# Performance work log

Hardware: AMD Instinct MI355X
Metric: run time of the kernel (lower is better)

Reference implementation:

```python
import jax, jax.numpy as jnp
import numpy as np

N = 16384      # nodes
E = 524288     # edges (avg degree 32)
F_IN = 128     # input features
H1 = 256       # first_gcn_dimensions
H2 = 256       # second_gcn_dimensions
D1 = 64        # first_dense_neurons
D2 = 2         # second_dense_neurons (fixed by EYE=ones(2))


def setup_inputs() -> dict:
    key = jax.random.key(0)
    ks = jax.random.split(key, 8)
    w = lambda k, shp: (jax.random.normal(k, shp, jnp.float32) * 0.05)
    return dict(
        features=jax.random.normal(ks[0], (N, F_IN), jnp.float32),
        edges=jax.random.randint(ks[1], (2, E), 0, N),
        W1=w(ks[2], (F_IN, H1)), b1=jnp.zeros((H1,), jnp.float32),
        W2=w(ks[3], (H1, H2)), b2=jnp.zeros((H2,), jnp.float32),
        fc1_w=w(ks[4], (D1, H2)), fc1_b=jnp.zeros((D1,), jnp.float32),
        fc2_w=w(ks[5], (D2, D1)), fc2_b=jnp.zeros((D2,), jnp.float32),
    )


def gcn_conv(x, W, b, src, dst, n):
    """PyG GCNConv: xW, add self-loops, symmetric D^-1/2 (A+I) D^-1/2 aggregation."""
    x = x @ W
    loops = jnp.arange(n)
    s = jnp.concatenate([src, loops])
    d = jnp.concatenate([dst, loops])
    deg = jax.ops.segment_sum(jnp.ones(s.shape, x.dtype), d, num_segments=n)
    dinv = jnp.where(deg > 0, jax.lax.rsqrt(deg), 0.0)
    msg = x[s] * (dinv[s] * dinv[d])[:, None]          # gather + scale
    return jax.ops.segment_sum(msg, d, num_segments=n) + b  # scatter-add


def reference(features, edges, W1, b1, W2, b2, fc1_w, fc1_b, fc2_w, fc2_b):
    n = features.shape[0]
    src, dst = edges[0], edges[1]
    h1 = jax.nn.relu(gcn_conv(features, W1, b1, src, dst, n))
    h2 = gcn_conv(h1, W2, b2, src, dst, n)                 # [N, H2]
    a1 = jnp.tanh(h2 @ fc1_w.T + fc1_b)                    # [N, D1]
    assignment = jax.nn.softmax(a1 @ fc2_w.T + fc2_b, axis=1)  # [N, 2]
    group_features = assignment.T @ h2                     # [2, H2]
    # to_dense_adj: dense NxN adjacency, duplicate edges accumulate
    adj = jnp.zeros((n, n), h2.dtype).at[src, dst].add(1.0)
    new_adj = assignment.T @ (adj @ assignment)            # [2, 2]
    positive = jnp.clip(group_features[0][None, :], -100.0, 100.0)
    negative = jnp.clip(group_features[1][None, :], -100.0, 100.0)
    # F.normalize(p=1, dim=1) with eps=1e-12
    denom = jnp.maximum(jnp.sum(jnp.abs(new_adj), axis=1, keepdims=True), 1e-12)
    norm_diag = jnp.diag(new_adj / denom)
    pos_penalty = jnp.mean((norm_diag - 1.0) ** 2)         # MSE vs ones(2)
    graph_embedding = jnp.mean(group_features, axis=0, keepdims=True)  # [1, H2]
    return (graph_embedding, positive, negative, pos_penalty)
```

## Files before the change

kernel.cpp:

```cpp
#include <hip/hip_runtime.h>
#include <hip/hip_bf16.h>
#include <math.h>

#define N_NODES 16384
#define N_EDGES 524288
#define F_IN 128
#define H1 256
#define H2 256
#define D1 64
#define NA_GRID 512
#define DEG_CAP 96

typedef __attribute__((ext_vector_type(8))) short short8;
typedef __attribute__((ext_vector_type(4))) float floatx4;
typedef unsigned short ushort_t;
typedef unsigned int uint_t;

__device__ inline float bf2f(ushort_t u) {
    union { uint_t i; float f; } v;
    v.i = ((uint_t)u) << 16;
    return v.f;
}
__device__ inline ushort_t f2bs(float x) {
    __hip_bfloat16 h = __float2bfloat16(x);
    return *reinterpret_cast<ushort_t*>(&h);
}

__global__ __launch_bounds__(256) void hist_kernel(
    const int* __restrict__ dst, int* __restrict__ cnt) {
    int e = blockIdx.x * 256 + threadIdx.x;
    atomicAdd(&cnt[dst[e]], 1);
}

__global__ __launch_bounds__(256) void prep_fill(
    const int* __restrict__ src, const int* __restrict__ dst,
    const float* __restrict__ features, const float* __restrict__ W1,
    const float* __restrict__ W2, const float* __restrict__ fc1_w,
    const int* __restrict__ cnt, int* __restrict__ cur,
    int* __restrict__ col, ushort_t* __restrict__ z,
    ushort_t* __restrict__ W1t, ushort_t* __restrict__ W2t,
    ushort_t* __restrict__ fc1bf, float* __restrict__ dinv) {
    int b = blockIdx.x, t = threadIdx.x;
    if (b < 2048) {
        int e = b * 256 + t;
        int d = dst[e];
        int pos = atomicAdd(&cur[d], 1);
        if (pos < DEG_CAP) col[d * DEG_CAP + pos] = src[e];
    } else if (b < 4096) {
        int idx = ((b - 2048) * 256 + t) * 4;
        float di = rsqrtf((float)(cnt[idx >> 7] + 1));
        float4 v = *(const float4*)&features[idx];
        uint_t lo = (uint_t)f2bs(v.x * di) | ((uint_t)f2bs(v.y * di) << 16);
        uint_t hi = (uint_t)f2bs(v.z * di) | ((uint_t)f2bs(v.w * di) << 16);
        uint2 p; p.x = lo; p.y = hi;
        *(uint2*)&z[idx] = p;
    } else if (b < 4224) {
        int idx = (b - 4096) * 256 + t;
        int n = idx >> 7, k = idx & 127;
        W1t[idx] = f2bs(W1[k * 256 + n]);
    } else if (b < 4480) {
        int idx = (b - 4224) * 256 + t;
        int n = idx >> 8, k = idx & 255;
        W2t[idx] = f2bs(W2[k * 256 + n]);
    } else if (b < 4544) {
        int idx = (b - 4480) * 256 + t;
        fc1bf[idx] = f2bs(fc1_w[idx]);
    } else {
        int n = (b - 4544) * 256 + t;
        dinv[n] = rsqrtf((float)(cnt[n] + 1));
    }
}

__global__ __launch_bounds__(256) void fused_layer1(
    const ushort_t* __restrict__ zfeat, const int* __restrict__ cnt,
    const int* __restrict__ col, const float* __restrict__ dinv,
    const float* __restrict__ b1, const ushort_t* __restrict__ W1t,
    const ushort_t* __restrict__ W2t, ushort_t* __restrict__ bufY) {
    __shared__ __align__(16) ushort_t Az[16 * 136];
    __shared__ __align__(16) ushort_t Ah[16 * 264];
    const int tid = threadIdx.x;
    const int lane = tid & 63;
    const int wave = tid >> 6;
    const int m = lane & 15;
    const int quad = lane >> 4;
    const int row0 = blockIdx.x * 16;

    for (int ii = 0; ii < 4; ++ii) {
        const int nl = wave * 4 + ii;
        const int node = __builtin_amdgcn_readfirstlane(row0 + nl);
        const int foff = lane * 2;
        uint_t self = *(const uint_t*)&zfeat[(size_t)node * 128 + foff];
        float a0 = bf2f((ushort_t)(self & 0xffff));
        float a1 = bf2f((ushort_t)(self >> 16));
        const int s0 = node * DEG_CAP;
        const int s1 = s0 + min(cnt[node], DEG_CAP);
        int base = s0;
        for (; base + 8 <= s1; base += 8) {
            uint_t uu[8];
            #pragma unroll
            for (int q = 0; q < 8; ++q) {
                int j = col[base + q];
                uu[q] = *(const uint_t*)&zfeat[(size_t)j * 128 + foff];
            }
            #pragma unroll
            for (int q = 0; q < 8; ++q) {
                a0 += bf2f((ushort_t)(uu[q] & 0xffff));
                a1 += bf2f((ushort_t)(uu[q] >> 16));
            }
        }
        for (; base < s1; ++base) {
            int j = col[base];
            uint_t u = *(const uint_t*)&zfeat[(size_t)j * 128 + foff];
            a0 += bf2f((ushort_t)(u & 0xffff));
            a1 += bf2f((ushort_t)(u >> 16));
        }
        float di = dinv[node];
        *(uint_t*)&Az[nl * 136 + foff] =
            (uint_t)f2bs(a0 * di) | ((uint_t)f2bs(a1 * di) << 16);
    }
    __syncthreads();

    const int wcol0 = wave * 64;
    floatx4 acc[4];
    const floatx4 zero4 = {0.f, 0.f, 0.f, 0.f};
    #pragma unroll
    for (int j = 0; j < 4; ++j) acc[j] = zero4;
    #pragma unroll
    for (int k0 = 0; k0 < 128; k0 += 32) {
        short8 a = *(const short8*)&Az[m * 136 + k0 + quad * 8];
        #pragma unroll
        for (int j = 0; j < 4; ++j) {
            short8 bb = *(const short8*)
                &W1t[(size_t)(wcol0 + j * 16 + m) * 128 + k0 + quad * 8];
            acc[j] = __builtin_amdgcn_mfma_f32_16x16x32_bf16(a, bb, acc[j], 0, 0, 0);
        }
    }
    #pragma unroll
    for (int j = 0; j < 4; ++j) {
        int cg = wcol0 + j * 16 + m;
        float bv = b1[cg];
        #pragma unroll
        for (int r = 0; r < 4; ++r) {
            float v = fmaxf(acc[j][r] + bv, 0.0f);
            Ah[(quad * 4 + r) * 264 + cg] = f2bs(v);
        }
    }
    __syncthreads();

    #pragma unroll
    for (int j = 0; j < 4; ++j) acc[j] = zero4;
    #pragma unroll
    for (int k0 = 0; k0 < 256; k0 += 32) {
        short8 a = *(const short8*)&Ah[m * 264 + k0 + quad * 8];
        #pragma unroll
        for (int j = 0; j < 4; ++j) {
            short8 bb = *(const short8*)
                &W2t[(size_t)(wcol0 + j * 16 + m) * 256 + k0 + quad * 8];
            acc[j] = __builtin_amdgcn_mfma_f32_16x16x32_bf16(a, bb, acc[j], 0, 0, 0);
        }
    }
    float rs4[4];
    #pragma unroll
    for (int r = 0; r < 4; ++r) rs4[r] = dinv[row0 + quad * 4 + r];
    #pragma unroll
    for (int j = 0; j < 4; ++j) {
        int cg = wcol0 + j * 16 + m;
        #pragma unroll
        for (int r = 0; r < 4; ++r)
            bufY[(size_t)(row0 + quad * 4 + r) * 256 + cg] = f2bs(acc[j][r] * rs4[r]);
    }
}

__global__ __launch_bounds__(256) void fused_assign(
    const ushort_t* __restrict__ bufY, const int* __restrict__ cnt,
    const int* __restrict__ col, const float* __restrict__ dinv,
    const float* __restrict__ b2, const ushort_t* __restrict__ fc1bf,
    const float* __restrict__ fc1_b, const float* __restrict__ fc2_w,
    const float* __restrict__ fc2_b, float* __restrict__ assign,
    float* __restrict__ gfr) {
    __shared__ __align__(16) ushort_t Ah[16 * 264];
    __shared__ float sha[16][65];
    __shared__ float sas0[16], sas1[16];
    const int tid = threadIdx.x;
    const int lane = tid & 63;
    const int wave = tid >> 6;
    const int m = lane & 15;
    const int quad = lane >> 4;
    const int row0 = blockIdx.x * 16;

    for (int ii = 0; ii < 4; ++ii) {
        const int nl = wave * 4 + ii;
        const int node = __builtin_amdgcn_readfirstlane(row0 + nl);
        const int foff = lane * 4;
        float a0, a1, a2, a3;
        {
            uint2 u = *(const uint2*)&bufY[(size_t)node * 256 + foff];
            a0 = bf2f((ushort_t)(u.x & 0xffff));
            a1 = bf2f((ushort_t)(u.x >> 16));
            a2 = bf2f((ushort_t)(u.y & 0xffff));
            a3 = bf2f((ushort_t)(u.y >> 16));
        }
        const int s0 = node * DEG_CAP;
        const int s1 = s0 + min(cnt[node], DEG_CAP);
        int base = s0;
        for (; base + 8 <= s1; base += 8) {
            uint2 uu[8];
            #pragma unroll
            for (int q = 0; q < 8; ++q) {
                int j = col[base + q];
                uu[q] = *(const uint2*)&bufY[(size_t)j * 256 + foff];
            }
            #pragma unroll
            for (int q = 0; q < 8; ++q) {
                a0 += bf2f((ushort_t)(uu[q].x & 0xffff));
                a1 += bf2f((ushort_t)(uu[q].x >> 16));
                a2 += bf2f((ushort_t)(uu[q].y & 0xffff));
                a3 += bf2f((ushort_t)(uu[q].y >> 16));
            }
        }
        for (; base < s1; ++base) {
            int j = col[base];
            uint2 u = *(const uint2*)&bufY[(size_t)j * 256 + foff];
            a0 += bf2f((ushort_t)(u.x & 0xffff));
            a1 += bf2f((ushort_t)(u.x >> 16));
            a2 += bf2f((ushort_t)(u.y & 0xffff));
            a3 += bf2f((ushort_t)(u.y >> 16));
        }
        float di = dinv[node];
        uint2 pk;
        pk.x = (uint_t)f2bs(a0 * di + b2[foff + 0]) |
               ((uint_t)f2bs(a1 * di + b2[foff + 1]) << 16);
        pk.y = (uint_t)f2bs(a2 * di + b2[foff + 2]) |
               ((uint_t)f2bs(a3 * di + b2[foff + 3]) << 16);
        *(uint2*)&Ah[nl * 264 + foff] = pk;
    }
    __syncthreads();

    floatx4 acc = {0.f, 0.f, 0.f, 0.f};
    #pragma unroll
    for (int k0 = 0; k0 < 256; k0 += 32) {
        short8 a = *(const short8*)&Ah[m * 264 + k0 + quad * 8];
        short8 bb = *(const short8*)
            &fc1bf[(size_t)(wave * 16 + m) * 256 + k0 + quad * 8];
        acc = __builtin_amdgcn_mfma_f32_16x16x32_bf16(a, bb, acc, 0, 0, 0);
    }
    {
        int cg = wave * 16 + m;
        float bv = fc1_b[cg];
        #pragma unroll
        for (int r = 0; r < 4; ++r)
            sha[quad * 4 + r][cg] = tanhf(acc[r] + bv);
    }
    __syncthreads();

    if (tid < 16) {
        float p0 = fc2_b[0], p1 = fc2_b[1];
        #pragma unroll 8
        for (int t = 0; t < 64; ++t) {
            float a = sha[tid][t];
            p0 += a * fc2_w[t];
            p1 += a * fc2_w[64 + t];
        }
        float mx = fmaxf(p0, p1);
        float e0 = expf(p0 - mx), e1 = expf(p1 - mx);
        float inv = 1.0f / (e0 + e1);
        float2 as; as.x = e0 * inv; as.y = e1 * inv;
        *(float2*)&assign[(row0 + tid) * 2] = as;
        sas0[tid] = as.x; sas1[tid] = as.y;
    }
    __syncthreads();

    float acc0 = 0.f, acc1 = 0.f;
    #pragma unroll
    for (int i = 0; i < 16; ++i) {
        float h = bf2f(Ah[i * 264 + tid]);
        acc0 += sas0[i] * h;
        acc1 += sas1[i] * h;
    }
    float* gfc = gfr + (blockIdx.x & 3) * 512;
    atomicAdd(&gfc[tid], acc0);
    atomicAdd(&gfc[256 + tid], acc1);
}

__global__ __launch_bounds__(256) void newadj_kernel(
    const int* __restrict__ src, const int* __restrict__ dst,
    const float* __restrict__ assign, float* __restrict__ napart) {
    __shared__ float red[4][4];
    const int tid = threadIdx.x;
    const int b = blockIdx.x;
    const int lane = tid & 63;
    const int wave = tid >> 6;

    float a00 = 0.f, a01 = 0.f, a10 = 0.f, a11 = 0.f;
    for (int e = b * 256 + tid; e < N_EDGES; e += NA_GRID * 256) {
        int s = src[e], d = dst[e];
        float s0 = assign[s * 2], s1 = assign[s * 2 + 1];
        float d0 = assign[d * 2], d1 = assign[d * 2 + 1];
        a00 += s0 * d0; a01 += s0 * d1; a10 += s1 * d0; a11 += s1 * d1;
    }
    #pragma unroll
    for (int off = 32; off; off >>= 1) {
        a00 += __shfl_down(a00, off);
        a01 += __shfl_down(a01, off);
        a10 += __shfl_down(a10, off);
        a11 += __shfl_down(a11, off);
    }
    if (lane == 0) {
        red[wave][0] = a00; red[wave][1] = a01;
        red[wave][2] = a10; red[wave][3] = a11;
    }
    __syncthreads();
    if (tid < 4) {
        float v = red[0][tid] + red[1][tid] + red[2][tid] + red[3][tid];
        napart[b * 4 + tid] = v;
    }
}

__global__ __launch_bounds__(256) void finalize_kernel(
    const float* __restrict__ gfr, const float* __restrict__ napart,
    float* __restrict__ out) {
    __shared__ float na[4];
    int t = threadIdx.x;
    int wave = t >> 6, lane = t & 63;
    float acc = 0.f;
    for (int i = lane; i < NA_GRID; i += 64) acc += napart[i * 4 + wave];
    #pragma unroll
    for (int off = 32; off; off >>= 1) acc += __shfl_down(acc, off);
    if (lane == 0) na[wave] = acc;
    __syncthreads();
    float g0 = gfr[t] + gfr[512 + t] + gfr[1024 + t] + gfr[1536 + t];
    float g1 = gfr[256 + t] + gfr[768 + t] + gfr[1280 + t] + gfr[1792 + t];
    out[t] = 0.5f * (g0 + g1);
    out[256 + t] = fminf(fmaxf(g0, -100.f), 100.f);
    out[512 + t] = fminf(fmaxf(g1, -100.f), 100.f);
    if (t == 0) {
        float n00 = na[0], n01 = na[1], n10 = na[2], n11 = na[3];
        float den0 = fmaxf(fabsf(n00) + fabsf(n01), 1e-12f);
        float den1 = fmaxf(fabsf(n10) + fabsf(n11), 1e-12f);
        float x0 = n00 / den0 - 1.0f;
        float x1 = n11 / den1 - 1.0f;
        out[768] = 0.5f * (x0 * x0 + x1 * x1);
    }
}


extern "C" void kernel_launch(void* const* d_in, const int* in_sizes, int n_in,
                              void* d_out, int out_size, void* d_ws, size_t ws_size,
                              hipStream_t stream) {
    const float* features = (const float*)d_in[0];
    const int* edges = (const int*)d_in[1];
    const int* src = edges;
    const int* dst = edges + N_EDGES;
    const float* W1 = (const float*)d_in[2];
    const float* b1 = (const float*)d_in[3];
    const float* W2 = (const float*)d_in[4];
    const float* b2 = (const float*)d_in[5];
    const float* fc1_w = (const float*)d_in[6];
    const float* fc1_b = (const float*)d_in[7];
    const float* fc2_w = (const float*)d_in[8];
    const float* fc2_b = (const float*)d_in[9];
    float* out = (float*)d_out;

    char* ws = (char*)d_ws;
    auto carve = [&](size_t bytes) {
        void* q = (void*)ws;
        ws += (bytes + 255) & ~(size_t)255;
        return q;
    };
    int* cnt = (int*)carve(N_NODES * 4);
    int* cur = (int*)carve(N_NODES * 4);
    float* gfr = (float*)carve(4 * 512 * 4);
    float* dinv = (float*)carve(N_NODES * 4);
    int* col = (int*)carve((size_t)N_NODES * DEG_CAP * 4);
    float* assign = (float*)carve(N_NODES * 2 * 4);
    float* napart = (float*)carve(NA_GRID * 4 * 4);
    ushort_t* fc1bf = (ushort_t*)carve(64 * 256 * 2);
    ushort_t* zfeat = (ushort_t*)carve((size_t)N_NODES * F_IN * 2);
    ushort_t* W1t = (ushort_t*)carve(256 * 128 * 2);
    ushort_t* W2t = (ushort_t*)carve(256 * 256 * 2);
    ushort_t* bufY = (ushort_t*)carve((size_t)N_NODES * 256 * 2);

    hipMemsetAsync(cnt, 0, N_NODES * 4 * 2 + 4 * 512 * 4, stream);

    hist_kernel<<<N_EDGES / 256, 256, 0, stream>>>(dst, cnt);
    prep_fill<<<4608, 256, 0, stream>>>(src, dst, features, W1, W2, fc1_w,
                                        cnt, cur, col, zfeat, W1t, W2t,
                                        fc1bf, dinv);
    fused_layer1<<<N_NODES / 16, 256, 0, stream>>>(
        zfeat, cnt, col, dinv, b1, W1t, W2t, bufY);
    fused_assign<<<N_NODES / 16, 256, 0, stream>>>(
        bufY, cnt, col, dinv, b2, fc1bf, fc1_b, fc2_w, fc2_b, assign, gfr);
    newadj_kernel<<<NA_GRID, 256, 0, stream>>>(src, dst, assign, napart);
    finalize_kernel<<<1, 256, 0, stream>>>(gfr, napart, out);
}
```

Measured before the change: 210.2 us.

## Drop histogram pass, compute dinv on the fly, fuse finalize via ticket

Removes the separate degree histogram kernel and reuses the CSR fill counter (cur) as the degree count. Features are no longer prescaled by dinv. Instead, layer 1 computes rsqrt(deg+1) per neighbour on the fly, which adds a random cnt gather per edge. The finalize kernel is folded into the new-adjacency kernel using a last-block ticket counter, and that kernel's grid is cut from 512 to 128 blocks. Together these save two launches and one pass over the edge list, at the cost of extra scattered loads in the layer-1 gather.

```diff
diff --git a/kernel.cpp b/kernel.cpp
--- a/kernel.cpp
+++ b/kernel.cpp
@@ -8,7 +8,7 @@
 #define H1 256
 #define H2 256
 #define D1 64
-#define NA_GRID 512
+#define NA_GRID 128
 #define DEG_CAP 96
 
 typedef __attribute__((ext_vector_type(8))) short short8;
@@ -26,20 +26,13 @@
     return *reinterpret_cast<ushort_t*>(&h);
 }
 
-__global__ __launch_bounds__(256) void hist_kernel(
-    const int* __restrict__ dst, int* __restrict__ cnt) {
-    int e = blockIdx.x * 256 + threadIdx.x;
-    atomicAdd(&cnt[dst[e]], 1);
-}
-
 __global__ __launch_bounds__(256) void prep_fill(
     const int* __restrict__ src, const int* __restrict__ dst,
     const float* __restrict__ features, const float* __restrict__ W1,
     const float* __restrict__ W2, const float* __restrict__ fc1_w,
-    const int* __restrict__ cnt, int* __restrict__ cur,
-    int* __restrict__ col, ushort_t* __restrict__ z,
+    int* __restrict__ cur, int* __restrict__ col, ushort_t* __restrict__ z,
     ushort_t* __restrict__ W1t, ushort_t* __restrict__ W2t,
-    ushort_t* __restrict__ fc1bf, float* __restrict__ dinv) {
+    ushort_t* __restrict__ fc1bf) {
     int b = blockIdx.x, t = threadIdx.x;
     if (b < 2048) {
         int e = b * 256 + t;
@@ -48,11 +41,10 @@
         if (pos < DEG_CAP) col[d * DEG_CAP + pos] = src[e];
     } else if (b < 4096) {
         int idx = ((b - 2048) * 256 + t) * 4;
-        float di = rsqrtf((float)(cnt[idx >> 7] + 1));
         float4 v = *(const float4*)&features[idx];
-        uint_t lo = (uint_t)f2bs(v.x * di) | ((uint_t)f2bs(v.y * di) << 16);
-        uint_t hi = (uint_t)f2bs(v.z * di) | ((uint_t)f2bs(v.w * di) << 16);
-        uint2 p; p.x = lo; p.y = hi;
+        uint2 p;
+        p.x = (uint_t)f2bs(v.x) | ((uint_t)f2bs(v.y) << 16);
+        p.y = (uint_t)f2bs(v.z) | ((uint_t)f2bs(v.w) << 16);
         *(uint2*)&z[idx] = p;
     } else if (b < 4224) {
         int idx = (b - 4096) * 256 + t;
@@ -62,20 +54,17 @@
         int idx = (b - 4224) * 256 + t;
         int n = idx >> 8, k = idx & 255;
         W2t[idx] = f2bs(W2[k * 256 + n]);
-    } else if (b < 4544) {
+    } else {
         int idx = (b - 4480) * 256 + t;
         fc1bf[idx] = f2bs(fc1_w[idx]);
-    } else {
-        int n = (b - 4544) * 256 + t;
-        dinv[n] = rsqrtf((float)(cnt[n] + 1));
     }
 }
 
 __global__ __launch_bounds__(256) void fused_layer1(
     const ushort_t* __restrict__ zfeat, const int* __restrict__ cnt,
-    const int* __restrict__ col, const float* __restrict__ dinv,
-    const float* __restrict__ b1, const ushort_t* __restrict__ W1t,
-    const ushort_t* __restrict__ W2t, ushort_t* __restrict__ bufY) {
+    const int* __restrict__ col, const float* __restrict__ b1,
+    const ushort_t* __restrict__ W1t, const ushort_t* __restrict__ W2t,
+    ushort_t* __restrict__ bufY) {
     __shared__ __align__(16) ushort_t Az[16 * 136];
     __shared__ __align__(16) ushort_t Ah[16 * 264];
     const int tid = threadIdx.x;
@@ -89,34 +78,37 @@
         const int nl = wave * 4 + ii;
         const int node = __builtin_amdgcn_readfirstlane(row0 + nl);
         const int foff = lane * 2;
+        const int deg = cnt[node];
+        float dnode = rsqrtf((float)(deg + 1));
         uint_t self = *(const uint_t*)&zfeat[(size_t)node * 128 + foff];
-        float a0 = bf2f((ushort_t)(self & 0xffff));
-        float a1 = bf2f((ushort_t)(self >> 16));
+        float a0 = dnode * bf2f((ushort_t)(self & 0xffff));
+        float a1 = dnode * bf2f((ushort_t)(self >> 16));
         const int s0 = node * DEG_CAP;
-        const int s1 = s0 + min(cnt[node], DEG_CAP);
+        const int s1 = s0 + min(deg, DEG_CAP);
         int base = s0;
         for (; base + 8 <= s1; base += 8) {
-            uint_t uu[8];
+            uint_t uu[8]; float dv[8];
             #pragma unroll
             for (int q = 0; q < 8; ++q) {
                 int j = col[base + q];
+                dv[q] = rsqrtf((float)(cnt[j] + 1));
                 uu[q] = *(const uint_t*)&zfeat[(size_t)j * 128 + foff];
             }
             #pragma unroll
             for (int q = 0; q < 8; ++q) {
-                a0 += bf2f((ushort_t)(uu[q] & 0xffff));
-                a1 += bf2f((ushort_t)(uu[q] >> 16));
+                a0 += dv[q] * bf2f((ushort_t)(uu[q] & 0xffff));
+                a1 += dv[q] * bf2f((ushort_t)(uu[q] >> 16));
             }
         }
         for (; base < s1; ++base) {
             int j = col[base];
+            float dv = rsqrtf((float)(cnt[j] + 1));
             uint_t u = *(const uint_t*)&zfeat[(size_t)j * 128 + foff];
-            a0 += bf2f((ushort_t)(u & 0xffff));
-            a1 += bf2f((ushort_t)(u >> 16));
-        }
-        float di = dinv[node];
+            a0 += dv * bf2f((ushort_t)(u & 0xffff));
+            a1 += dv * bf2f((ushort_t)(u >> 16));
+        }
         *(uint_t*)&Az[nl * 136 + foff] =
-            (uint_t)f2bs(a0 * di) | ((uint_t)f2bs(a1 * di) << 16);
+            (uint_t)f2bs(a0 * dnode) | ((uint_t)f2bs(a1 * dnode) << 16);
     }
     __syncthreads();
 
@@ -161,7 +153,8 @@
     }
     float rs4[4];
     #pragma unroll
-    for (int r = 0; r < 4; ++r) rs4[r] = dinv[row0 + quad * 4 + r];
+    for (int r = 0; r < 4; ++r)
+        rs4[r] = rsqrtf((float)(cnt[row0 + quad * 4 + r] + 1));
     #pragma unroll
     for (int j = 0; j < 4; ++j) {
         int cg = wcol0 + j * 16 + m;
@@ -173,11 +166,10 @@
 
 __global__ __launch_bounds__(256) void fused_assign(
     const ushort_t* __restrict__ bufY, const int* __restrict__ cnt,
-    const int* __restrict__ col, const float* __restrict__ dinv,
-    const float* __restrict__ b2, const ushort_t* __restrict__ fc1bf,
-    const float* __restrict__ fc1_b, const float* __restrict__ fc2_w,
-    const float* __restrict__ fc2_b, float* __restrict__ assign,
-    float* __restrict__ gfr) {
+    const int* __restrict__ col, const float* __restrict__ b2,
+    const ushort_t* __restrict__ fc1bf, const float* __restrict__ fc1_b,
+    const float* __restrict__ fc2_w, const float* __restrict__ fc2_b,
+    float* __restrict__ assign, float* __restrict__ gfr) {
     __shared__ __align__(16) ushort_t Ah[16 * 264];
     __shared__ float sha[16][65];
     __shared__ float sas0[16], sas1[16];
@@ -192,6 +184,7 @@
         const int nl = wave * 4 + ii;
         const int node = __builtin_amdgcn_readfirstlane(row0 + nl);
         const int foff = lane * 4;
+        const int deg = cnt[node];
         float a0, a1, a2, a3;
         {
             uint2 u = *(const uint2*)&bufY[(size_t)node * 256 + foff];
@@ -201,7 +194,7 @@
             a3 = bf2f((ushort_t)(u.y >> 16));
         }
         const int s0 = node * DEG_CAP;
-        const int s1 = s0 + min(cnt[node], DEG_CAP);
+        const int s1 = s0 + min(deg, DEG_CAP);
         int base = s0;
         for (; base + 8 <= s1; base += 8) {
             uint2 uu[8];
@@ -226,7 +219,7 @@
             a2 += bf2f((ushort_t)(u.y & 0xffff));
             a3 += bf2f((ushort_t)(u.y >> 16));
         }
-        float di = dinv[node];
+        float di = rsqrtf((float)(deg + 1));
         uint2 pk;
         pk.x = (uint_t)f2bs(a0 * di + b2[foff + 0]) |
                ((uint_t)f2bs(a1 * di + b2[foff + 1]) << 16);
@@ -282,10 +275,13 @@
     atomicAdd(&gfc[256 + tid], acc1);
 }
 
-__global__ __launch_bounds__(256) void newadj_kernel(
+__global__ __launch_bounds__(256) void newadj_fin(
     const int* __restrict__ src, const int* __restrict__ dst,
-    const float* __restrict__ assign, float* __restrict__ napart) {
+    const float* __restrict__ assign, float* __restrict__ napart,
+    int* __restrict__ cntt, const float* __restrict__ gfr,
+    float* __restrict__ out) {
     __shared__ float red[4][4];
+    __shared__ int sticket;
     const int tid = threadIdx.x;
     const int b = blockIdx.x;
     const int lane = tid & 63;
@@ -312,28 +308,31 @@
     __syncthreads();
     if (tid < 4) {
         float v = red[0][tid] + red[1][tid] + red[2][tid] + red[3][tid];
-        napart[b * 4 + tid] = v;
-    }
-}
-
-__global__ __launch_bounds__(256) void finalize_kernel(
-    const float* __restrict__ gfr, const float* __restrict__ napart,
-    float* __restrict__ out) {
+        __hip_atomic_store(&napart[b * 4 + tid], v, __ATOMIC_RELEASE,
+                           __HIP_MEMORY_SCOPE_AGENT);
+    }
+    __syncthreads();
+    if (tid == 0)
+        sticket = __hip_atomic_fetch_add(cntt, 1, __ATOMIC_ACQ_REL,
+                                         __HIP_MEMORY_SCOPE_AGENT);
+    __syncthreads();
+    if (sticket != NA_GRID - 1) return;
+
+    float acc = 0.f;
+    for (int i = lane; i < NA_GRID; i += 64)
+        acc += __hip_atomic_load(&napart[i * 4 + wave], __ATOMIC_RELAXED,
+                                 __HIP_MEMORY_SCOPE_AGENT);
+    #pragma unroll
+    for (int off = 32; off; off >>= 1) acc += __shfl_down(acc, off);
     __shared__ float na[4];
-    int t = threadIdx.x;
-    int wave = t >> 6, lane = t & 63;
-    float acc = 0.f;
-    for (int i = lane; i < NA_GRID; i += 64) acc += napart[i * 4 + wave];
-    #pragma unroll
-    for (int off = 32; off; off >>= 1) acc += __shfl_down(acc, off);
     if (lane == 0) na[wave] = acc;
     __syncthreads();
-    float g0 = gfr[t] + gfr[512 + t] + gfr[1024 + t] + gfr[1536 + t];
-    float g1 = gfr[256 + t] + gfr[768 + t] + gfr[1280 + t] + gfr[1792 + t];
-    out[t] = 0.5f * (g0 + g1);
-    out[256 + t] = fminf(fmaxf(g0, -100.f), 100.f);
-    out[512 + t] = fminf(fmaxf(g1, -100.f), 100.f);
-    if (t == 0) {
+    float g0 = gfr[tid] + gfr[512 + tid] + gfr[1024 + tid] + gfr[1536 + tid];
+    float g1 = gfr[256 + tid] + gfr[768 + tid] + gfr[1280 + tid] + gfr[1792 + tid];
+    out[tid] = 0.5f * (g0 + g1);
+    out[256 + tid] = fminf(fmaxf(g0, -100.f), 100.f);
+    out[512 + tid] = fminf(fmaxf(g1, -100.f), 100.f);
+    if (tid == 0) {
         float n00 = na[0], n01 = na[1], n10 = na[2], n11 = na[3];
         float den0 = fmaxf(fabsf(n00) + fabsf(n01), 1e-12f);
         float den1 = fmaxf(fabsf(n10) + fabsf(n11), 1e-12f);
@@ -367,10 +366,9 @@
         ws += (bytes + 255) & ~(size_t)255;
         return q;
     };
-    int* cnt = (int*)carve(N_NODES * 4);
     int* cur = (int*)carve(N_NODES * 4);
     float* gfr = (float*)carve(4 * 512 * 4);
-    float* dinv = (float*)carve(N_NODES * 4);
+    int* cnt_na = (int*)carve(256);
     int* col = (int*)carve((size_t)N_NODES * DEG_CAP * 4);
     float* assign = (float*)carve(N_NODES * 2 * 4);
     float* napart = (float*)carve(NA_GRID * 4 * 4);
@@ -380,16 +378,14 @@
     ushort_t* W2t = (ushort_t*)carve(256 * 256 * 2);
     ushort_t* bufY = (ushort_t*)carve((size_t)N_NODES * 256 * 2);
 
-    hipMemsetAsync(cnt, 0, N_NODES * 4 * 2 + 4 * 512 * 4, stream);
-
-    hist_kernel<<<N_EDGES / 256, 256, 0, stream>>>(dst, cnt);
-    prep_fill<<<4608, 256, 0, stream>>>(src, dst, features, W1, W2, fc1_w,
-                                        cnt, cur, col, zfeat, W1t, W2t,
-                                        fc1bf, dinv);
+    hipMemsetAsync(cur, 0, N_NODES * 4 + 4 * 512 * 4 + 256, stream);
+
+    prep_fill<<<4544, 256, 0, stream>>>(src, dst, features, W1, W2, fc1_w,
+                                        cur, col, zfeat, W1t, W2t, fc1bf);
     fused_layer1<<<N_NODES / 16, 256, 0, stream>>>(
-        zfeat, cnt, col, dinv, b1, W1t, W2t, bufY);
+        zfeat, cur, col, b1, W1t, W2t, bufY);
     fused_assign<<<N_NODES / 16, 256, 0, stream>>>(
-        bufY, cnt, col, dinv, b2, fc1bf, fc1_b, fc2_w, fc2_b, assign, gfr);
-    newadj_kernel<<<NA_GRID, 256, 0, stream>>>(src, dst, assign, napart);
-    finalize_kernel<<<1, 256, 0, stream>>>(gfr, napart, out);
-}
+        bufY, cur, col, b2, fc1bf, fc1_b, fc2_w, fc2_b, assign, gfr);
+    newadj_fin<<<NA_GRID, 256, 0, stream>>>(src, dst, assign, napart,
+                                            cnt_na, gfr, out);
+}
```

New measurement: 209.6 us. About the same (-0.3%).
